# Kernel tuning notes

Hardware: AMD Instinct MI355X
Metric: run time of the kernel (lower is better)

The kernel has to match this reference:

```python
import jax, jax.numpy as jnp
import numpy as np

N_NODES = 50000
N_EDGES = 800000
D = 64
H = 4
EPS = 1e-5  # BatchNorm1d default eps


def setup_inputs() -> dict:
    key = jax.random.key(0)
    k1, k2, k3, k4, k5 = jax.random.split(key, 5)
    return {
        "h": jax.random.normal(k1, (N_NODES, D), dtype=jnp.float32),
        "e": jax.random.normal(k2, (N_EDGES, D), dtype=jnp.float32),
        "norm": jax.random.uniform(k3, (N_NODES, 1), dtype=jnp.float32),
        "gamma": jnp.ones((H, D), dtype=jnp.float32),
        "beta": jnp.zeros((H, D), dtype=jnp.float32),
        "src": jax.random.randint(k4, (N_EDGES,), 0, N_NODES, dtype=jnp.int32),
        "dst": jax.random.randint(k5, (N_EDGES,), 0, N_NODES, dtype=jnp.int32),
    }


def _segment_softmax(scores, seg, n):
    # numerically-stable softmax over incoming edges of each dst node
    m = jax.ops.segment_max(scores, seg, num_segments=n)
    m = jnp.where(jnp.isfinite(m), m, 0.0)  # empty segments -> 0
    ex = jnp.exp(scores - m[seg])
    denom = jax.ops.segment_sum(ex, seg, num_segments=n)
    return ex / denom[seg]


def reference(h, e, norm, gamma, beta, src, dst):
    z = h * norm  # [N, D]
    # edge attention score: dot(z_src, z_dst), then attn activation (relu)
    z_src = z[src]  # [E, D]
    scores = jax.nn.relu(jnp.sum(z_src * z[dst], axis=-1))  # [E]
    # segment softmax over mailbox (incoming edges per dst node)
    alpha = _segment_softmax(scores, dst, N_NODES)  # [E]
    # weighted scatter-sum aggregation (identical across heads: no per-head proj)
    agg = jax.ops.segment_sum(alpha[:, None] * z_src, dst, num_segments=N_NODES)  # [N, D]
    # BatchNorm1d in training mode (biased variance), per-head affine
    mean = jnp.mean(agg, axis=0)
    var = jnp.var(agg, axis=0)
    xhat = (agg - mean) / jnp.sqrt(var + EPS)  # [N, D]
    # per-head: gamma*xhat + beta -> relu -> * norm ; then concat over heads
    heads = jax.nn.relu(gamma[:, None, :] * xhat[None] + beta[:, None, :]) * norm[None]  # [H, N, D]
    h_out = jnp.transpose(heads, (1, 0, 2)).reshape(N_NODES, H * D)
    return h_out, e
```

## Files before the change

kernel.cpp:

```cpp
#include <hip/hip_runtime.h>
#include <hip/hip_bf16.h>

#define BLK 256
static constexpr float EPS = 1e-5f;
static constexpr int CAP = 64;

typedef float f32x4 __attribute__((ext_vector_type(4)));

__device__ inline unsigned short f2bf(float f) {
  unsigned int u = __float_as_uint(f);
  return (unsigned short)((u + 0x7fffu + ((u >> 16) & 1u)) >> 16);
}
__device__ inline unsigned int pack2(float lo, float hi) {
  return (unsigned int)f2bf(lo) | ((unsigned int)f2bf(hi) << 16);
}
__device__ inline float blo(unsigned int u) { return __uint_as_float(u << 16); }
__device__ inline float bhi(unsigned int u) { return __uint_as_float(u & 0xffff0000u); }

__device__ inline void do_copy(const f32x4* __restrict__ s, f32x4* __restrict__ d,
                               int lo, int hi, int tid, int nthr) {
  int i = lo + tid;
  for (; i + 3 * nthr < hi; i += 4 * nthr) {
    f32x4 v0 = __builtin_nontemporal_load(&s[i]);
    f32x4 v1 = __builtin_nontemporal_load(&s[i + nthr]);
    f32x4 v2 = __builtin_nontemporal_load(&s[i + 2 * nthr]);
    f32x4 v3 = __builtin_nontemporal_load(&s[i + 3 * nthr]);
    __builtin_nontemporal_store(v0, &d[i]);
    __builtin_nontemporal_store(v1, &d[i + nthr]);
    __builtin_nontemporal_store(v2, &d[i + 2 * nthr]);
    __builtin_nontemporal_store(v3, &d[i + 3 * nthr]);
  }
  for (; i < hi; i += nthr) {
    f32x4 v = __builtin_nontemporal_load(&s[i]);
    __builtin_nontemporal_store(v, &d[i]);
  }
}

__global__ void k_prep(const float* __restrict__ hbuf, const float* __restrict__ norm,
                       uint4* __restrict__ z, int n8, int* __restrict__ cursor,
                       float* __restrict__ sums, int nNodes,
                       const f32x4* __restrict__ esrc, f32x4* __restrict__ edst,
                       int cLo, int cHi, int ncopy) {
  int b = blockIdx.x;
  if (b < ncopy) {
    do_copy(esrc, edst, cLo, cHi, b * BLK + (int)threadIdx.x, ncopy * BLK);
    return;
  }
  int i = (b - ncopy) * BLK + threadIdx.x;
  if (i < nNodes) cursor[i] = 0;
  if (i < 128) sums[i] = 0.f;
  if (i >= n8) return;
  float s = norm[i >> 3];
  const float4* hp = reinterpret_cast<const float4*>(hbuf) + (size_t)i * 2;
  float4 a = hp[0], bb = hp[1];
  uint4 o;
  o.x = pack2(a.x * s, a.y * s);
  o.y = pack2(a.z * s, a.w * s);
  o.z = pack2(bb.x * s, bb.y * s);
  o.w = pack2(bb.z * s, bb.w * s);
  z[i] = o;
}

__global__ void k_scat(const int* __restrict__ src, const int* __restrict__ dst,
                       int* __restrict__ cursor, int* __restrict__ csr, int nE,
                       const f32x4* __restrict__ esrc, f32x4* __restrict__ edst,
                       int cLo, int cHi, int ncopy) {
  int b = blockIdx.x;
  if (b < ncopy) {
    do_copy(esrc, edst, cLo, cHi, b * BLK + (int)threadIdx.x, ncopy * BLK);
    return;
  }
  int e = (b - ncopy) * BLK + threadIdx.x;
  if (e >= nE) return;
  int d = dst[e];
  int slot = atomicAdd(&cursor[d], 1);
  if (slot < CAP) csr[d * CAP + slot] = src[e];
}

__global__ void k_fused(const uint4* __restrict__ z4, const int* __restrict__ cursor,
                        const int* __restrict__ csr, float4* __restrict__ agg4, int n,
                        const f32x4* __restrict__ esrc, f32x4* __restrict__ edst,
                        int cLo, int cHi, int ncopy) {
  int b = blockIdx.x;
  if (b < ncopy) {
    do_copy(esrc, edst, cLo, cHi, b * BLK + (int)threadIdx.x, ncopy * BLK);
    return;
  }
  int w = (b - ncopy) * (BLK / 64) + ((int)threadIdx.x >> 6);
  if (w >= n) return;
  int lane = threadIdx.x & 63;
  int sub = lane & 7, grp = lane >> 3;
  int cnt = min(cursor[w], CAP);
  int beg = w * CAP;

  uint4 zd = z4[(size_t)w * 8 + sub];
  float d0 = blo(zd.x), d1 = bhi(zd.x), d2 = blo(zd.y), d3 = bhi(zd.y);
  float d4 = blo(zd.z), d5 = bhi(zd.z), d6 = blo(zd.w), d7 = bhi(zd.w);

  float dsum = 0.f;
  float acc0 = 0.f, acc1 = 0.f, acc2 = 0.f, acc3 = 0.f;
  float acc4 = 0.f, acc5 = 0.f, acc6 = 0.f, acc7 = 0.f;

  for (int base = 0; base < cnt; base += 8) {
    int j = base + grp;
    bool valid = (j < cnt);
    int sj = valid ? csr[beg + j] : 0;
    uint4 au = z4[(size_t)sj * 8 + sub];
    float a0 = blo(au.x), a1 = bhi(au.x), a2 = blo(au.y), a3 = bhi(au.y);
    float a4 = blo(au.z), a5 = bhi(au.z), a6 = blo(au.w), a7 = bhi(au.w);
    float p = a0 * d0;
    p = fmaf(a1, d1, p); p = fmaf(a2, d2, p); p = fmaf(a3, d3, p);
    p = fmaf(a4, d4, p); p = fmaf(a5, d5, p); p = fmaf(a6, d6, p);
    p = fmaf(a7, d7, p);
    p += __shfl_xor(p, 1);
    p += __shfl_xor(p, 2);
    p += __shfl_xor(p, 4);
    p = fmaxf(p, 0.f);
    float wv = valid ? __expf(p - 64.f) : 0.f;
    dsum += wv;
    acc0 = fmaf(wv, a0, acc0); acc1 = fmaf(wv, a1, acc1);
    acc2 = fmaf(wv, a2, acc2); acc3 = fmaf(wv, a3, acc3);
    acc4 = fmaf(wv, a4, acc4); acc5 = fmaf(wv, a5, acc5);
    acc6 = fmaf(wv, a6, acc6); acc7 = fmaf(wv, a7, acc7);
  }
  #pragma unroll
  for (int off = 8; off < 64; off <<= 1) {
    dsum += __shfl_xor(dsum, off);
    acc0 += __shfl_xor(acc0, off); acc1 += __shfl_xor(acc1, off);
    acc2 += __shfl_xor(acc2, off); acc3 += __shfl_xor(acc3, off);
    acc4 += __shfl_xor(acc4, off); acc5 += __shfl_xor(acc5, off);
    acc6 += __shfl_xor(acc6, off); acc7 += __shfl_xor(acc7, off);
  }
  float inv = (dsum > 0.f) ? 1.0f / dsum : 0.f;
  if (grp == 0) {
    agg4[(size_t)w * 16 + sub * 2 + 0] =
        make_float4(acc0 * inv, acc1 * inv, acc2 * inv, acc3 * inv);
    agg4[(size_t)w * 16 + sub * 2 + 1] =
        make_float4(acc4 * inv, acc5 * inv, acc6 * inv, acc7 * inv);
  }
}

__global__ void k_stats(const float* __restrict__ agg, float* __restrict__ sums, int n) {
  __shared__ float ls[128];
  if (threadIdx.x < 128) ls[threadIdx.x] = 0.f;
  __syncthreads();
  int col = threadIdx.x & 63;
  int rq  = threadIdx.x >> 6;
  int rend = min(n, (int)(blockIdx.x + 1) * 256);
  float s = 0.f, s2 = 0.f;
  for (int r = blockIdx.x * 256 + rq; r < rend; r += 4) {
    float v = agg[(size_t)r * 64 + col];
    s += v; s2 += v * v;
  }
  atomicAdd(&ls[col], s);
  atomicAdd(&ls[64 + col], s2);
  __syncthreads();
  if (threadIdx.x < 128) unsafeAtomicAdd(&sums[threadIdx.x], ls[threadIdx.x]);
}

__global__ void k_out(const float* __restrict__ agg, const float* __restrict__ sums,
                      const float* __restrict__ gamma, const float* __restrict__ beta,
                      const float* __restrict__ norm, f32x4* __restrict__ out, int n64,
                      float invN) {
  __shared__ float4 sm4[16], si4[16];
  float* sm = (float*)sm4;
  float* si = (float*)si4;
  if (threadIdx.x < 64) {
    float mu = sums[threadIdx.x] * invN;
    sm[threadIdx.x] = mu;
    si[threadIdx.x] = rsqrtf(sums[64 + threadIdx.x] * invN - mu * mu + EPS);
  }
  __syncthreads();
  int g = blockIdx.x * BLK + threadIdx.x;
  if (g >= n64) return;
  int node = g >> 6, within = g & 63;
  int head = within >> 4, d4 = within & 15;
  float4 a  = reinterpret_cast<const float4*>(agg)[(size_t)node * 16 + d4];
  float4 mu = sm4[d4];
  float4 iv = si4[d4];
  float4 ga = reinterpret_cast<const float4*>(gamma)[head * 16 + d4];
  float4 be = reinterpret_cast<const float4*>(beta)[head * 16 + d4];
  float s = norm[node];
  f32x4 r;
  r.x = fmaxf(fmaf(ga.x, (a.x - mu.x) * iv.x, be.x), 0.f) * s;
  r.y = fmaxf(fmaf(ga.y, (a.y - mu.y) * iv.y, be.y), 0.f) * s;
  r.z = fmaxf(fmaf(ga.z, (a.z - mu.z) * iv.z, be.z), 0.f) * s;
  r.w = fmaxf(fmaf(ga.w, (a.w - mu.w) * iv.w, be.w), 0.f) * s;
  __builtin_nontemporal_store(r, &out[g]);
}

__global__ void k_tail(const f32x4* __restrict__ esrc, f32x4* __restrict__ edst, int n4) {
  do_copy(esrc, edst, 0, n4, blockIdx.x * BLK + (int)threadIdx.x, gridDim.x * BLK);
}

extern "C" void kernel_launch(void* const* d_in, const int* in_sizes, int n_in,
                              void* d_out, int out_size, void* d_ws, size_t ws_size,
                              hipStream_t stream) {
  const float* h     = (const float*)d_in[0];
  const float* e     = (const float*)d_in[1];
  const float* norm  = (const float*)d_in[2];
  const float* gamma = (const float*)d_in[3];
  const float* beta  = (const float*)d_in[4];
  const int*   src   = (const int*)d_in[5];
  const int*   dst   = (const int*)d_in[6];
  const int N = in_sizes[2];
  const int E = in_sizes[5];
  float* out = (float*)d_out;

  float* eout = out + (size_t)N * 256;
  size_t eBytes = (size_t)E * 64 * sizeof(float);

  size_t need = 0;
  auto sz = [&](size_t b) { size_t o = need; need += (b + 255) & ~(size_t)255; return o; };
  size_t oZ    = sz((size_t)N * 64 * sizeof(unsigned short));
  size_t oAgg  = sz((size_t)N * 64 * sizeof(float));
  size_t oCsr  = sz((size_t)N * CAP * sizeof(int));
  size_t oCur  = sz((size_t)N * sizeof(int));
  size_t oSums = sz(128 * sizeof(float));

  bool useWs = (ws_size >= need);
  char* scratch = useWs ? (char*)d_ws : ((char*)eout + (eBytes - need));

  uint4* z      = (uint4*)(scratch + oZ);
  float* agg    = (float*)(scratch + oAgg);
  int*   csr    = (int*)  (scratch + oCsr);
  int*   cursor = (int*)  (scratch + oCur);
  float* sums   = (float*)(scratch + oSums);

  size_t headBytes = useWs ? eBytes : (eBytes - need);
  int headF4 = (int)(headBytes / 16);
  int tailF4 = (int)((eBytes - headBytes) / 16);

  int c1 = (int)((size_t)headF4 * 25 / 100) & ~15;
  int c2 = (int)((size_t)headF4 * 55 / 100) & ~15;

  int n8 = N * 8;
  int zzB = (n8 + BLK - 1) / BLK;
  const int NC1 = 512, NC2 = 512, NC3 = 768;

  k_prep<<<NC1 + zzB, BLK, 0, stream>>>(h, norm, z, n8, cursor, sums, N,
                                        (const f32x4*)e, (f32x4*)eout, 0, c1, NC1);

  int scB = (E + BLK - 1) / BLK;
  k_scat<<<NC2 + scB, BLK, 0, stream>>>(src, dst, cursor, csr, E,
                                        (const f32x4*)e, (f32x4*)eout, c1, c2, NC2);

  int ndB = (N + 3) / 4;
  k_fused<<<NC3 + ndB, BLK, 0, stream>>>(z, cursor, csr, (float4*)agg, N,
                                         (const f32x4*)e, (f32x4*)eout, c2, headF4, NC3);

  k_stats<<<(N + 255) / 256, 256, 0, stream>>>(agg, sums, N);

  int n64 = N * 64;
  k_out<<<(n64 + BLK - 1) / BLK, BLK, 0, stream>>>(agg, sums, gamma, beta, norm,
                                                   (f32x4*)out, n64, 1.0f / (float)N);

  if (tailF4 > 0)
    k_tail<<<1024, BLK, 0, stream>>>((const f32x4*)e + headF4, (f32x4*)eout + headF4,
                                     tailF4);
}
```

Baseline: 168.8 us.

## Interleave edge-feature copy into every compute block and store CSR indices as 16-bit

The pass-through copy of the edge features used to run on dedicated extra copy blocks in the first three kernels. It now runs inside every compute block of all five kernels, with each block copying a contiguous chunk before doing its own work. The split points are retuned so the stats and output kernels also carry part of the copy. CSR neighbor indices are stored as unsigned short, which halves scatter-write and gather-read traffic but only holds while node ids fit in 16 bits. Putting the copy in front of the compute in each block may delay the compute work rather than overlap with it.

After: 190.7 us. +13.0%, slower.

```diff
diff --git a/kernel.cpp b/kernel.cpp
--- a/kernel.cpp
+++ b/kernel.cpp
@@ -17,20 +17,14 @@
 __device__ inline float blo(unsigned int u) { return __uint_as_float(u << 16); }
 __device__ inline float bhi(unsigned int u) { return __uint_as_float(u & 0xffff0000u); }
 
-__device__ inline void do_copy(const f32x4* __restrict__ s, f32x4* __restrict__ d,
-                               int lo, int hi, int tid, int nthr) {
-  int i = lo + tid;
-  for (; i + 3 * nthr < hi; i += 4 * nthr) {
-    f32x4 v0 = __builtin_nontemporal_load(&s[i]);
-    f32x4 v1 = __builtin_nontemporal_load(&s[i + nthr]);
-    f32x4 v2 = __builtin_nontemporal_load(&s[i + 2 * nthr]);
-    f32x4 v3 = __builtin_nontemporal_load(&s[i + 3 * nthr]);
-    __builtin_nontemporal_store(v0, &d[i]);
-    __builtin_nontemporal_store(v1, &d[i + nthr]);
-    __builtin_nontemporal_store(v2, &d[i + 2 * nthr]);
-    __builtin_nontemporal_store(v3, &d[i + 3 * nthr]);
-  }
-  for (; i < hi; i += nthr) {
+__device__ inline void block_copy(const f32x4* __restrict__ s, f32x4* __restrict__ d,
+                                  int cLo, int cHi) {
+  int total = cHi - cLo;
+  if (total <= 0) return;
+  int per = (total + (int)gridDim.x - 1) / (int)gridDim.x;
+  int lo = cLo + (int)blockIdx.x * per;
+  int hi = min(cHi, lo + per);
+  for (int i = lo + (int)threadIdx.x; i < hi; i += BLK) {
     f32x4 v = __builtin_nontemporal_load(&s[i]);
     __builtin_nontemporal_store(v, &d[i]);
   }
@@ -40,13 +34,9 @@
                        uint4* __restrict__ z, int n8, int* __restrict__ cursor,
                        float* __restrict__ sums, int nNodes,
                        const f32x4* __restrict__ esrc, f32x4* __restrict__ edst,
-                       int cLo, int cHi, int ncopy) {
-  int b = blockIdx.x;
-  if (b < ncopy) {
-    do_copy(esrc, edst, cLo, cHi, b * BLK + (int)threadIdx.x, ncopy * BLK);
-    return;
-  }
-  int i = (b - ncopy) * BLK + threadIdx.x;
+                       int cLo, int cHi) {
+  block_copy(esrc, edst, cLo, cHi);
+  int i = blockIdx.x * BLK + threadIdx.x;
   if (i < nNodes) cursor[i] = 0;
   if (i < 128) sums[i] = 0.f;
   if (i >= n8) return;
@@ -62,31 +52,23 @@
 }
 
 __global__ void k_scat(const int* __restrict__ src, const int* __restrict__ dst,
-                       int* __restrict__ cursor, int* __restrict__ csr, int nE,
+                       int* __restrict__ cursor, unsigned short* __restrict__ csr, int nE,
                        const f32x4* __restrict__ esrc, f32x4* __restrict__ edst,
-                       int cLo, int cHi, int ncopy) {
-  int b = blockIdx.x;
-  if (b < ncopy) {
-    do_copy(esrc, edst, cLo, cHi, b * BLK + (int)threadIdx.x, ncopy * BLK);
-    return;
-  }
-  int e = (b - ncopy) * BLK + threadIdx.x;
+                       int cLo, int cHi) {
+  block_copy(esrc, edst, cLo, cHi);
+  int e = blockIdx.x * BLK + threadIdx.x;
   if (e >= nE) return;
   int d = dst[e];
   int slot = atomicAdd(&cursor[d], 1);
-  if (slot < CAP) csr[d * CAP + slot] = src[e];
+  if (slot < CAP) csr[d * CAP + slot] = (unsigned short)src[e];
 }
 
 __global__ void k_fused(const uint4* __restrict__ z4, const int* __restrict__ cursor,
-                        const int* __restrict__ csr, float4* __restrict__ agg4, int n,
-                        const f32x4* __restrict__ esrc, f32x4* __restrict__ edst,
-                        int cLo, int cHi, int ncopy) {
-  int b = blockIdx.x;
-  if (b < ncopy) {
-    do_copy(esrc, edst, cLo, cHi, b * BLK + (int)threadIdx.x, ncopy * BLK);
-    return;
-  }
-  int w = (b - ncopy) * (BLK / 64) + ((int)threadIdx.x >> 6);
+                        const unsigned short* __restrict__ csr, float4* __restrict__ agg4,
+                        int n, const f32x4* __restrict__ esrc, f32x4* __restrict__ edst,
+                        int cLo, int cHi) {
+  block_copy(esrc, edst, cLo, cHi);
+  int w = blockIdx.x * (BLK / 64) + ((int)threadIdx.x >> 6);
   if (w >= n) return;
   int lane = threadIdx.x & 63;
   int sub = lane & 7, grp = lane >> 3;
@@ -104,7 +86,7 @@
   for (int base = 0; base < cnt; base += 8) {
     int j = base + grp;
     bool valid = (j < cnt);
-    int sj = valid ? csr[beg + j] : 0;
+    int sj = valid ? (int)csr[beg + j] : 0;
     uint4 au = z4[(size_t)sj * 8 + sub];
     float a0 = blo(au.x), a1 = bhi(au.x), a2 = blo(au.y), a3 = bhi(au.y);
     float a4 = blo(au.z), a5 = bhi(au.z), a6 = blo(au.w), a7 = bhi(au.w);
@@ -140,7 +122,10 @@
   }
 }
 
-__global__ void k_stats(const float* __restrict__ agg, float* __restrict__ sums, int n) {
+__global__ void k_stats(const float* __restrict__ agg, float* __restrict__ sums, int n,
+                        const f32x4* __restrict__ esrc, f32x4* __restrict__ edst,
+                        int cLo, int cHi) {
+  block_copy(esrc, edst, cLo, cHi);
   __shared__ float ls[128];
   if (threadIdx.x < 128) ls[threadIdx.x] = 0.f;
   __syncthreads();
@@ -161,7 +146,9 @@
 __global__ void k_out(const float* __restrict__ agg, const float* __restrict__ sums,
                       const float* __restrict__ gamma, const float* __restrict__ beta,
                       const float* __restrict__ norm, f32x4* __restrict__ out, int n64,
-                      float invN) {
+                      float invN, const f32x4* __restrict__ esrc,
+                      f32x4* __restrict__ edst, int cLo, int cHi) {
+  block_copy(esrc, edst, cLo, cHi);
   __shared__ float4 sm4[16], si4[16];
   float* sm = (float*)sm4;
   float* si = (float*)si4;
@@ -190,7 +177,12 @@
 }
 
 __global__ void k_tail(const f32x4* __restrict__ esrc, f32x4* __restrict__ edst, int n4) {
-  do_copy(esrc, edst, 0, n4, blockIdx.x * BLK + (int)threadIdx.x, gridDim.x * BLK);
+  int tid = blockIdx.x * BLK + threadIdx.x;
+  int stride = gridDim.x * BLK;
+  for (int i = tid; i < n4; i += stride) {
+    f32x4 v = __builtin_nontemporal_load(&esrc[i]);
+    __builtin_nontemporal_store(v, &edst[i]);
+  }
 }
 
 extern "C" void kernel_launch(void* const* d_in, const int* in_sizes, int n_in,
@@ -214,48 +206,48 @@
   auto sz = [&](size_t b) { size_t o = need; need += (b + 255) & ~(size_t)255; return o; };
   size_t oZ    = sz((size_t)N * 64 * sizeof(unsigned short));
   size_t oAgg  = sz((size_t)N * 64 * sizeof(float));
-  size_t oCsr  = sz((size_t)N * CAP * sizeof(int));
+  size_t oCsr  = sz((size_t)N * CAP * sizeof(unsigned short));
   size_t oCur  = sz((size_t)N * sizeof(int));
   size_t oSums = sz(128 * sizeof(float));
 
   bool useWs = (ws_size >= need);
   char* scratch = useWs ? (char*)d_ws : ((char*)eout + (eBytes - need));
 
-  uint4* z      = (uint4*)(scratch + oZ);
-  float* agg    = (float*)(scratch + oAgg);
-  int*   csr    = (int*)  (scratch + oCsr);
-  int*   cursor = (int*)  (scratch + oCur);
-  float* sums   = (float*)(scratch + oSums);
+  uint4*          z      = (uint4*)(scratch + oZ);
+  float*          agg    = (float*)(scratch + oAgg);
+  unsigned short* csr    = (unsigned short*)(scratch + oCsr);
+  int*            cursor = (int*)(scratch + oCur);
+  float*          sums   = (float*)(scratch + oSums);
 
   size_t headBytes = useWs ? eBytes : (eBytes - need);
   int headF4 = (int)(headBytes / 16);
   int tailF4 = (int)((eBytes - headBytes) / 16);
 
-  int c1 = (int)((size_t)headF4 * 25 / 100) & ~15;
-  int c2 = (int)((size_t)headF4 * 55 / 100) & ~15;
+  int b1 = (int)((size_t)headF4 * 20 / 100) & ~15;
+  int b2 = (int)((size_t)headF4 * 40 / 100) & ~15;
+  int b3 = (int)((size_t)headF4 * 85 / 100) & ~15;
+  int b4 = (int)((size_t)headF4 * 90 / 100) & ~15;
+
+  const f32x4* e4   = (const f32x4*)e;
+  f32x4*       eo4  = (f32x4*)eout;
 
   int n8 = N * 8;
-  int zzB = (n8 + BLK - 1) / BLK;
-  const int NC1 = 512, NC2 = 512, NC3 = 768;
-
-  k_prep<<<NC1 + zzB, BLK, 0, stream>>>(h, norm, z, n8, cursor, sums, N,
-                                        (const f32x4*)e, (f32x4*)eout, 0, c1, NC1);
-
-  int scB = (E + BLK - 1) / BLK;
-  k_scat<<<NC2 + scB, BLK, 0, stream>>>(src, dst, cursor, csr, E,
-                                        (const f32x4*)e, (f32x4*)eout, c1, c2, NC2);
+  k_prep<<<(n8 + BLK - 1) / BLK, BLK, 0, stream>>>(h, norm, z, n8, cursor, sums, N,
+                                                   e4, eo4, 0, b1);
+
+  k_scat<<<(E + BLK - 1) / BLK, BLK, 0, stream>>>(src, dst, cursor, csr, E,
+                                                  e4, eo4, b1, b2);
 
   int ndB = (N + 3) / 4;
-  k_fused<<<NC3 + ndB, BLK, 0, stream>>>(z, cursor, csr, (float4*)agg, N,
-                                         (const f32x4*)e, (f32x4*)eout, c2, headF4, NC3);
-
-  k_stats<<<(N + 255) / 256, 256, 0, stream>>>(agg, sums, N);
+  k_fused<<<ndB, BLK, 0, stream>>>(z, cursor, csr, (float4*)agg, N, e4, eo4, b2, b3);
+
+  k_stats<<<(N + 255) / 256, 256, 0, stream>>>(agg, sums, N, e4, eo4, b3, b4);
 
   int n64 = N * 64;
   k_out<<<(n64 + BLK - 1) / BLK, BLK, 0, stream>>>(agg, sums, gamma, beta, norm,
-                                                   (f32x4*)out, n64, 1.0f / (float)N);
+                                                   (f32x4*)out, n64, 1.0f / (float)N,
+                                                   e4, eo4, b4, headF4);
 
   if (tailF4 > 0)
-    k_tail<<<1024, BLK, 0, stream>>>((const f32x4*)e + headF4, (f32x4*)eout + headF4,
-                                     tailF4);
-}
+    k_tail<<<1024, BLK, 0, stream>>>(e4 + headF4, eo4 + headF4, tailF4);
+}
```

## Store CSR indices as 16-bit and spread the edge copy across all kernels

Applied to the files above, without the earlier changes.

Neighbour indices in the CSR buffer are stored as unsigned short instead of int, halving CSR write and read traffic. The passthrough copy of the edge tensor is redistributed so k_stats and k_out also carry copy blocks, with most of it (10%-90%) placed alongside the fused gather kernel. Node ids go up to 49999, which fits in 16 bits, so the narrowing only holds while N stays at or below 65536 and silently breaks for larger graphs.

New measurement: 193.2 us. 1.14x slower.

```diff
diff --git a/kernel.cpp b/kernel.cpp
--- a/kernel.cpp
+++ b/kernel.cpp
@@ -62,7 +62,7 @@
 }
 
 __global__ void k_scat(const int* __restrict__ src, const int* __restrict__ dst,
-                       int* __restrict__ cursor, int* __restrict__ csr, int nE,
+                       int* __restrict__ cursor, unsigned short* __restrict__ csr, int nE,
                        const f32x4* __restrict__ esrc, f32x4* __restrict__ edst,
                        int cLo, int cHi, int ncopy) {
   int b = blockIdx.x;
@@ -74,12 +74,12 @@
   if (e >= nE) return;
   int d = dst[e];
   int slot = atomicAdd(&cursor[d], 1);
-  if (slot < CAP) csr[d * CAP + slot] = src[e];
+  if (slot < CAP) csr[d * CAP + slot] = (unsigned short)src[e];
 }
 
 __global__ void k_fused(const uint4* __restrict__ z4, const int* __restrict__ cursor,
-                        const int* __restrict__ csr, float4* __restrict__ agg4, int n,
-                        const f32x4* __restrict__ esrc, f32x4* __restrict__ edst,
+                        const unsigned short* __restrict__ csr, float4* __restrict__ agg4,
+                        int n, const f32x4* __restrict__ esrc, f32x4* __restrict__ edst,
                         int cLo, int cHi, int ncopy) {
   int b = blockIdx.x;
   if (b < ncopy) {
@@ -104,7 +104,7 @@
   for (int base = 0; base < cnt; base += 8) {
     int j = base + grp;
     bool valid = (j < cnt);
-    int sj = valid ? csr[beg + j] : 0;
+    int sj = valid ? (int)csr[beg + j] : 0;
     uint4 au = z4[(size_t)sj * 8 + sub];
     float a0 = blo(au.x), a1 = bhi(au.x), a2 = blo(au.y), a3 = bhi(au.y);
     float a4 = blo(au.z), a5 = bhi(au.z), a6 = blo(au.w), a7 = bhi(au.w);
@@ -140,15 +140,23 @@
   }
 }
 
-__global__ void k_stats(const float* __restrict__ agg, float* __restrict__ sums, int n) {
+__global__ void k_stats(const float* __restrict__ agg, float* __restrict__ sums, int n,
+                        const f32x4* __restrict__ esrc, f32x4* __restrict__ edst,
+                        int cLo, int cHi, int ncopy) {
+  int b = blockIdx.x;
+  if (b < ncopy) {
+    do_copy(esrc, edst, cLo, cHi, b * BLK + (int)threadIdx.x, ncopy * BLK);
+    return;
+  }
   __shared__ float ls[128];
   if (threadIdx.x < 128) ls[threadIdx.x] = 0.f;
   __syncthreads();
+  int bid = b - ncopy;
   int col = threadIdx.x & 63;
   int rq  = threadIdx.x >> 6;
-  int rend = min(n, (int)(blockIdx.x + 1) * 256);
+  int rend = min(n, (bid + 1) * 256);
   float s = 0.f, s2 = 0.f;
-  for (int r = blockIdx.x * 256 + rq; r < rend; r += 4) {
+  for (int r = bid * 256 + rq; r < rend; r += 4) {
     float v = agg[(size_t)r * 64 + col];
     s += v; s2 += v * v;
   }
@@ -161,7 +169,13 @@
 __global__ void k_out(const float* __restrict__ agg, const float* __restrict__ sums,
                       const float* __restrict__ gamma, const float* __restrict__ beta,
                       const float* __restrict__ norm, f32x4* __restrict__ out, int n64,
-                      float invN) {
+                      float invN, const f32x4* __restrict__ esrc,
+                      f32x4* __restrict__ edst, int cLo, int cHi, int ncopy) {
+  int b = blockIdx.x;
+  if (b < ncopy) {
+    do_copy(esrc, edst, cLo, cHi, b * BLK + (int)threadIdx.x, ncopy * BLK);
+    return;
+  }
   __shared__ float4 sm4[16], si4[16];
   float* sm = (float*)sm4;
   float* si = (float*)si4;
@@ -171,7 +185,7 @@
     si[threadIdx.x] = rsqrtf(sums[64 + threadIdx.x] * invN - mu * mu + EPS);
   }
   __syncthreads();
-  int g = blockIdx.x * BLK + threadIdx.x;
+  int g = (b - ncopy) * BLK + threadIdx.x;
   if (g >= n64) return;
   int node = g >> 6, within = g & 63;
   int head = within >> 4, d4 = within & 15;
@@ -214,48 +228,54 @@
   auto sz = [&](size_t b) { size_t o = need; need += (b + 255) & ~(size_t)255; return o; };
   size_t oZ    = sz((size_t)N * 64 * sizeof(unsigned short));
   size_t oAgg  = sz((size_t)N * 64 * sizeof(float));
-  size_t oCsr  = sz((size_t)N * CAP * sizeof(int));
+  size_t oCsr  = sz((size_t)N * CAP * sizeof(unsigned short));
   size_t oCur  = sz((size_t)N * sizeof(int));
   size_t oSums = sz(128 * sizeof(float));
 
   bool useWs = (ws_size >= need);
   char* scratch = useWs ? (char*)d_ws : ((char*)eout + (eBytes - need));
 
-  uint4* z      = (uint4*)(scratch + oZ);
-  float* agg    = (float*)(scratch + oAgg);
-  int*   csr    = (int*)  (scratch + oCsr);
-  int*   cursor = (int*)  (scratch + oCur);
-  float* sums   = (float*)(scratch + oSums);
+  uint4*          z      = (uint4*)(scratch + oZ);
+  float*          agg    = (float*)(scratch + oAgg);
+  unsigned short* csr    = (unsigned short*)(scratch + oCsr);
+  int*            cursor = (int*)(scratch + oCur);
+  float*          sums   = (float*)(scratch + oSums);
 
   size_t headBytes = useWs ? eBytes : (eBytes - need);
   int headF4 = (int)(headBytes / 16);
   int tailF4 = (int)((eBytes - headBytes) / 16);
 
-  int c1 = (int)((size_t)headF4 * 25 / 100) & ~15;
-  int c2 = (int)((size_t)headF4 * 55 / 100) & ~15;
+  int c1 = (int)((size_t)headF4 *  5 / 100) & ~15;
+  int c2 = (int)((size_t)headF4 * 10 / 100) & ~15;
+  int c3 = (int)((size_t)headF4 * 90 / 100) & ~15;
+  int c4 = (int)((size_t)headF4 * 95 / 100) & ~15;
+
+  const f32x4* e4  = (const f32x4*)e;
+  f32x4*       eo4 = (f32x4*)eout;
+
+  const int NC1 = 256, NC2 = 256, NC3 = 1024, NC4 = 128, NC5 = 256;
 
   int n8 = N * 8;
   int zzB = (n8 + BLK - 1) / BLK;
-  const int NC1 = 512, NC2 = 512, NC3 = 768;
-
   k_prep<<<NC1 + zzB, BLK, 0, stream>>>(h, norm, z, n8, cursor, sums, N,
-                                        (const f32x4*)e, (f32x4*)eout, 0, c1, NC1);
+                                        e4, eo4, 0, c1, NC1);
 
   int scB = (E + BLK - 1) / BLK;
   k_scat<<<NC2 + scB, BLK, 0, stream>>>(src, dst, cursor, csr, E,
-                                        (const f32x4*)e, (f32x4*)eout, c1, c2, NC2);
+                                        e4, eo4, c1, c2, NC2);
 
   int ndB = (N + 3) / 4;
   k_fused<<<NC3 + ndB, BLK, 0, stream>>>(z, cursor, csr, (float4*)agg, N,
-                                         (const f32x4*)e, (f32x4*)eout, c2, headF4, NC3);
-
-  k_stats<<<(N + 255) / 256, 256, 0, stream>>>(agg, sums, N);
+                                         e4, eo4, c2, c3, NC3);
+
+  int stB = (N + 255) / 256;
+  k_stats<<<NC4 + stB, 256, 0, stream>>>(agg, sums, N, e4, eo4, c3, c4, NC4);
 
   int n64 = N * 64;
-  k_out<<<(n64 + BLK - 1) / BLK, BLK, 0, stream>>>(agg, sums, gamma, beta, norm,
-                                                   (f32x4*)out, n64, 1.0f / (float)N);
+  int outB = (n64 + BLK - 1) / BLK;
+  k_out<<<NC5 + outB, BLK, 0, stream>>>(agg, sums, gamma, beta, norm, (f32x4*)out,
+                                        n64, 1.0f / (float)N, e4, eo4, c4, headF4, NC5);
 
   if (tailF4 > 0)
-    k_tail<<<1024, BLK, 0, stream>>>((const f32x4*)e + headF4, (f32x4*)eout + headF4,
-                                     tailF4);
-}
+    k_tail<<<1024, BLK, 0, stream>>>(e4 + headF4, eo4 + headF4, tailF4);
+}
```

## Fuse BatchNorm statistics into aggregation kernel and spread edge copy into output kernel

Applied to the files above, without the earlier changes.

Per-column sum and sum-of-squares are now accumulated in shared memory inside the fused aggregation kernel as each node's output is written. This removes the separate stats kernel and its full re-read of the aggregated matrix. The passthrough copy of the edge tensor is also re-split across four kernels, so the output kernel carries a share of it too. The cost is many shared-memory atomics per node in the aggregation kernel and an extra barrier per block.

Result: slower. 433.2 us (+156.7%).

```diff
diff --git a/kernel.cpp b/kernel.cpp
--- a/kernel.cpp
+++ b/kernel.cpp
@@ -78,7 +78,8 @@
 }
 
 __global__ void k_fused(const uint4* __restrict__ z4, const int* __restrict__ cursor,
-                        const int* __restrict__ csr, float4* __restrict__ agg4, int n,
+                        const int* __restrict__ csr, float4* __restrict__ agg4,
+                        float* __restrict__ sums, int n,
                         const f32x4* __restrict__ esrc, f32x4* __restrict__ edst,
                         int cLo, int cHi, int ncopy) {
   int b = blockIdx.x;
@@ -86,82 +87,86 @@
     do_copy(esrc, edst, cLo, cHi, b * BLK + (int)threadIdx.x, ncopy * BLK);
     return;
   }
+  __shared__ float shbuf[128];
+  if (threadIdx.x < 128) shbuf[threadIdx.x] = 0.f;
+  __syncthreads();
+
   int w = (b - ncopy) * (BLK / 64) + ((int)threadIdx.x >> 6);
-  if (w >= n) return;
   int lane = threadIdx.x & 63;
   int sub = lane & 7, grp = lane >> 3;
-  int cnt = min(cursor[w], CAP);
-  int beg = w * CAP;
-
-  uint4 zd = z4[(size_t)w * 8 + sub];
-  float d0 = blo(zd.x), d1 = bhi(zd.x), d2 = blo(zd.y), d3 = bhi(zd.y);
-  float d4 = blo(zd.z), d5 = bhi(zd.z), d6 = blo(zd.w), d7 = bhi(zd.w);
-
-  float dsum = 0.f;
-  float acc0 = 0.f, acc1 = 0.f, acc2 = 0.f, acc3 = 0.f;
-  float acc4 = 0.f, acc5 = 0.f, acc6 = 0.f, acc7 = 0.f;
-
-  for (int base = 0; base < cnt; base += 8) {
-    int j = base + grp;
-    bool valid = (j < cnt);
-    int sj = valid ? csr[beg + j] : 0;
-    uint4 au = z4[(size_t)sj * 8 + sub];
-    float a0 = blo(au.x), a1 = bhi(au.x), a2 = blo(au.y), a3 = bhi(au.y);
-    float a4 = blo(au.z), a5 = bhi(au.z), a6 = blo(au.w), a7 = bhi(au.w);
-    float p = a0 * d0;
-    p = fmaf(a1, d1, p); p = fmaf(a2, d2, p); p = fmaf(a3, d3, p);
-    p = fmaf(a4, d4, p); p = fmaf(a5, d5, p); p = fmaf(a6, d6, p);
-    p = fmaf(a7, d7, p);
-    p += __shfl_xor(p, 1);
-    p += __shfl_xor(p, 2);
-    p += __shfl_xor(p, 4);
-    p = fmaxf(p, 0.f);
-    float wv = valid ? __expf(p - 64.f) : 0.f;
-    dsum += wv;
-    acc0 = fmaf(wv, a0, acc0); acc1 = fmaf(wv, a1, acc1);
-    acc2 = fmaf(wv, a2, acc2); acc3 = fmaf(wv, a3, acc3);
-    acc4 = fmaf(wv, a4, acc4); acc5 = fmaf(wv, a5, acc5);
-    acc6 = fmaf(wv, a6, acc6); acc7 = fmaf(wv, a7, acc7);
-  }
-  #pragma unroll
-  for (int off = 8; off < 64; off <<= 1) {
-    dsum += __shfl_xor(dsum, off);
-    acc0 += __shfl_xor(acc0, off); acc1 += __shfl_xor(acc1, off);
-    acc2 += __shfl_xor(acc2, off); acc3 += __shfl_xor(acc3, off);
-    acc4 += __shfl_xor(acc4, off); acc5 += __shfl_xor(acc5, off);
-    acc6 += __shfl_xor(acc6, off); acc7 += __shfl_xor(acc7, off);
-  }
-  float inv = (dsum > 0.f) ? 1.0f / dsum : 0.f;
-  if (grp == 0) {
-    agg4[(size_t)w * 16 + sub * 2 + 0] =
-        make_float4(acc0 * inv, acc1 * inv, acc2 * inv, acc3 * inv);
-    agg4[(size_t)w * 16 + sub * 2 + 1] =
-        make_float4(acc4 * inv, acc5 * inv, acc6 * inv, acc7 * inv);
-  }
-}
-
-__global__ void k_stats(const float* __restrict__ agg, float* __restrict__ sums, int n) {
-  __shared__ float ls[128];
-  if (threadIdx.x < 128) ls[threadIdx.x] = 0.f;
+  if (w < n) {
+    int cnt = min(cursor[w], CAP);
+    int beg = w * CAP;
+
+    uint4 zd = z4[(size_t)w * 8 + sub];
+    float d0 = blo(zd.x), d1 = bhi(zd.x), d2 = blo(zd.y), d3 = bhi(zd.y);
+    float d4 = blo(zd.z), d5 = bhi(zd.z), d6 = blo(zd.w), d7 = bhi(zd.w);
+
+    float dsum = 0.f;
+    float acc0 = 0.f, acc1 = 0.f, acc2 = 0.f, acc3 = 0.f;
+    float acc4 = 0.f, acc5 = 0.f, acc6 = 0.f, acc7 = 0.f;
+
+    for (int base = 0; base < cnt; base += 8) {
+      int j = base + grp;
+      bool valid = (j < cnt);
+      int sj = valid ? csr[beg + j] : 0;
+      uint4 au = z4[(size_t)sj * 8 + sub];
+      float a0 = blo(au.x), a1 = bhi(au.x), a2 = blo(au.y), a3 = bhi(au.y);
+      float a4 = blo(au.z), a5 = bhi(au.z), a6 = blo(au.w), a7 = bhi(au.w);
+      float p = a0 * d0;
+      p = fmaf(a1, d1, p); p = fmaf(a2, d2, p); p = fmaf(a3, d3, p);
+      p = fmaf(a4, d4, p); p = fmaf(a5, d5, p); p = fmaf(a6, d6, p);
+      p = fmaf(a7, d7, p);
+      p += __shfl_xor(p, 1);
+      p += __shfl_xor(p, 2);
+      p += __shfl_xor(p, 4);
+      p = fmaxf(p, 0.f);
+      float wv = valid ? __expf(p - 64.f) : 0.f;
+      dsum += wv;
+      acc0 = fmaf(wv, a0, acc0); acc1 = fmaf(wv, a1, acc1);
+      acc2 = fmaf(wv, a2, acc2); acc3 = fmaf(wv, a3, acc3);
+      acc4 = fmaf(wv, a4, acc4); acc5 = fmaf(wv, a5, acc5);
+      acc6 = fmaf(wv, a6, acc6); acc7 = fmaf(wv, a7, acc7);
+    }
+    #pragma unroll
+    for (int off = 8; off < 64; off <<= 1) {
+      dsum += __shfl_xor(dsum, off);
+      acc0 += __shfl_xor(acc0, off); acc1 += __shfl_xor(acc1, off);
+      acc2 += __shfl_xor(acc2, off); acc3 += __shfl_xor(acc3, off);
+      acc4 += __shfl_xor(acc4, off); acc5 += __shfl_xor(acc5, off);
+      acc6 += __shfl_xor(acc6, off); acc7 += __shfl_xor(acc7, off);
+    }
+    float inv = (dsum > 0.f) ? 1.0f / dsum : 0.f;
+    if (grp == 0) {
+      float v0 = acc0 * inv, v1 = acc1 * inv, v2 = acc2 * inv, v3 = acc3 * inv;
+      float v4 = acc4 * inv, v5 = acc5 * inv, v6 = acc6 * inv, v7 = acc7 * inv;
+      agg4[(size_t)w * 16 + sub * 2 + 0] = make_float4(v0, v1, v2, v3);
+      agg4[(size_t)w * 16 + sub * 2 + 1] = make_float4(v4, v5, v6, v7);
+      int c = sub * 8;
+      atomicAdd(&shbuf[c + 0], v0); atomicAdd(&shbuf[64 + c + 0], v0 * v0);
+      atomicAdd(&shbuf[c + 1], v1); atomicAdd(&shbuf[64 + c + 1], v1 * v1);
+      atomicAdd(&shbuf[c + 2], v2); atomicAdd(&shbuf[64 + c + 2], v2 * v2);
+      atomicAdd(&shbuf[c + 3], v3); atomicAdd(&shbuf[64 + c + 3], v3 * v3);
+      atomicAdd(&shbuf[c + 4], v4); atomicAdd(&shbuf[64 + c + 4], v4 * v4);
+      atomicAdd(&shbuf[c + 5], v5); atomicAdd(&shbuf[64 + c + 5], v5 * v5);
+      atomicAdd(&shbuf[c + 6], v6); atomicAdd(&shbuf[64 + c + 6], v6 * v6);
+      atomicAdd(&shbuf[c + 7], v7); atomicAdd(&shbuf[64 + c + 7], v7 * v7);
+    }
+  }
   __syncthreads();
-  int col = threadIdx.x & 63;
-  int rq  = threadIdx.x >> 6;
-  int rend = min(n, (int)(blockIdx.x + 1) * 256);
-  float s = 0.f, s2 = 0.f;
-  for (int r = blockIdx.x * 256 + rq; r < rend; r += 4) {
-    float v = agg[(size_t)r * 64 + col];
-    s += v; s2 += v * v;
-  }
-  atomicAdd(&ls[col], s);
-  atomicAdd(&ls[64 + col], s2);
-  __syncthreads();
-  if (threadIdx.x < 128) unsafeAtomicAdd(&sums[threadIdx.x], ls[threadIdx.x]);
+  if (threadIdx.x < 128) unsafeAtomicAdd(&sums[threadIdx.x], shbuf[threadIdx.x]);
 }
 
 __global__ void k_out(const float* __restrict__ agg, const float* __restrict__ sums,
                       const float* __restrict__ gamma, const float* __restrict__ beta,
                       const float* __restrict__ norm, f32x4* __restrict__ out, int n64,
-                      float invN) {
+                      float invN, const f32x4* __restrict__ esrc,
+                      f32x4* __restrict__ edst, int cLo, int cHi, int ncopy) {
+  int b = blockIdx.x;
+  if (b < ncopy) {
+    do_copy(esrc, edst, cLo, cHi, b * BLK + (int)threadIdx.x, ncopy * BLK);
+    return;
+  }
   __shared__ float4 sm4[16], si4[16];
   float* sm = (float*)sm4;
   float* si = (float*)si4;
@@ -171,7 +176,7 @@
     si[threadIdx.x] = rsqrtf(sums[64 + threadIdx.x] * invN - mu * mu + EPS);
   }
   __syncthreads();
-  int g = blockIdx.x * BLK + threadIdx.x;
+  int g = (b - ncopy) * BLK + threadIdx.x;
   if (g >= n64) return;
   int node = g >> 6, within = g & 63;
   int head = within >> 4, d4 = within & 15;
@@ -231,31 +236,33 @@
   int headF4 = (int)(headBytes / 16);
   int tailF4 = (int)((eBytes - headBytes) / 16);
 
-  int c1 = (int)((size_t)headF4 * 25 / 100) & ~15;
-  int c2 = (int)((size_t)headF4 * 55 / 100) & ~15;
+  int c1 = (int)((size_t)headF4 * 20 / 100) & ~15;
+  int c2 = (int)((size_t)headF4 * 45 / 100) & ~15;
+  int c3 = (int)((size_t)headF4 * 85 / 100) & ~15;
+
+  const f32x4* e4  = (const f32x4*)e;
+  f32x4*       eo4 = (f32x4*)eout;
+
+  const int NC1 = 512, NC2 = 512, NC3 = 768, NC4 = 256;
 
   int n8 = N * 8;
   int zzB = (n8 + BLK - 1) / BLK;
-  const int NC1 = 512, NC2 = 512, NC3 = 768;
-
   k_prep<<<NC1 + zzB, BLK, 0, stream>>>(h, norm, z, n8, cursor, sums, N,
-                                        (const f32x4*)e, (f32x4*)eout, 0, c1, NC1);
+                                        e4, eo4, 0, c1, NC1);
 
   int scB = (E + BLK - 1) / BLK;
   k_scat<<<NC2 + scB, BLK, 0, stream>>>(src, dst, cursor, csr, E,
-                                        (const f32x4*)e, (f32x4*)eout, c1, c2, NC2);
+                                        e4, eo4, c1, c2, NC2);
 
   int ndB = (N + 3) / 4;
-  k_fused<<<NC3 + ndB, BLK, 0, stream>>>(z, cursor, csr, (float4*)agg, N,
-                                         (const f32x4*)e, (f32x4*)eout, c2, headF4, NC3);
-
-  k_stats<<<(N + 255) / 256, 256, 0, stream>>>(agg, sums, N);
+  k_fused<<<NC3 + ndB, BLK, 0, stream>>>(z, cursor, csr, (float4*)agg, sums, N,
+                                         e4, eo4, c2, c3, NC3);
 
   int n64 = N * 64;
-  k_out<<<(n64 + BLK - 1) / BLK, BLK, 0, stream>>>(agg, sums, gamma, beta, norm,
-                                                   (f32x4*)out, n64, 1.0f / (float)N);
+  int outB = (n64 + BLK - 1) / BLK;
+  k_out<<<NC4 + outB, BLK, 0, stream>>>(agg, sums, gamma, beta, norm, (f32x4*)out,
+                                        n64, 1.0f / (float)N, e4, eo4, c3, headF4, NC4);
 
   if (tailF4 > 0)
-    k_tail<<<1024, BLK, 0, stream>>>((const f32x4*)e + headF4, (f32x4*)eout + headF4,
-                                     tailF4);
-}
+    k_tail<<<1024, BLK, 0, stream>>>(e4 + headF4, eo4 + headF4, tailF4);
+}
```
